# Kernel tuning notes

Measured on AMD Instinct MI355X. Metric: run time of the kernel, lower is better.

## Reference

```python
import jax, jax.numpy as jnp
import numpy as np

NE, NPER = 100000, 50000        # empresa / persona node counts
D_EMP, D_PER = 64, 32           # raw feature dims
H, OUT = 128, 64                # hidden_channels, out_channels
E_EE, E_PE, E_EP = 1600000, 800000, 800000
NEG_SLOPE = 0.2                 # GATConv leaky_relu slope


def setup_inputs() -> dict:
    key = jax.random.key(0)
    ks = jax.random.split(key, 40)

    def w(k, fi, fo):
        return jax.random.normal(k, (fi, fo), jnp.float32) / jnp.sqrt(jnp.float32(fi))

    def b(k, n):
        return jax.random.normal(k, (n,), jnp.float32) * 0.02

    return {
        "x_emp": jax.random.normal(ks[0], (NE, D_EMP), jnp.float32),
        "x_per": jax.random.normal(ks[1], (NPER, D_PER), jnp.float32),
        "ee_src": jax.random.randint(ks[2], (E_EE,), 0, NE, jnp.int32),
        "ee_dst": jax.random.randint(ks[3], (E_EE,), 0, NE, jnp.int32),
        "pe_src": jax.random.randint(ks[4], (E_PE,), 0, NPER, jnp.int32),
        "pe_dst": jax.random.randint(ks[5], (E_PE,), 0, NE, jnp.int32),
        "ep_src": jax.random.randint(ks[6], (E_EP,), 0, NE, jnp.int32),
        "ep_dst": jax.random.randint(ks[7], (E_EP,), 0, NPER, jnp.int32),
        # per-node-type input projections
        "lin_emp_w": w(ks[8], D_EMP, H), "lin_emp_b": b(ks[9], H),
        "lin_per_w": w(ks[10], D_PER, H), "lin_per_b": b(ks[11], H),
        # conv1: SAGEConv per edge type (H -> H)
        "s1_ee_Wl": w(ks[12], H, H), "s1_ee_bl": b(ks[13], H), "s1_ee_Wr": w(ks[14], H, H),
        "s1_pe_Wl": w(ks[15], H, H), "s1_pe_bl": b(ks[16], H), "s1_pe_Wr": w(ks[17], H, H),
        "s1_ep_Wl": w(ks[18], H, H), "s1_ep_bl": b(ks[19], H), "s1_ep_Wr": w(ks[20], H, H),
        # conv2: GATConv on empresa->empresa (H -> OUT, heads=1)
        "gat_Wsrc": w(ks[21], H, OUT), "gat_Wdst": w(ks[22], H, OUT),
        "gat_asrc": b(ks[23], OUT), "gat_adst": b(ks[24], OUT), "gat_b": b(ks[25], OUT),
        # conv2: SAGEConv on remaining edge types (H -> OUT)
        "s2_pe_Wl": w(ks[26], H, OUT), "s2_pe_bl": b(ks[27], OUT), "s2_pe_Wr": w(ks[28], H, OUT),
        "s2_ep_Wl": w(ks[29], H, OUT), "s2_ep_bl": b(ks[30], OUT), "s2_ep_Wr": w(ks[31], H, OUT),
    }


def _sage(h_src, h_dst, src, dst, Wl, bl, Wr, n_dst):
    # SAGEConv: mean-aggregate neighbor features, then lin_l(agg) + lin_r(x_dst)
    agg = jax.ops.segment_sum(h_src[src], dst, num_segments=n_dst)
    cnt = jax.ops.segment_sum(jnp.ones((src.shape[0], 1), h_src.dtype), dst,
                              num_segments=n_dst)
    mean = agg / jnp.maximum(cnt, 1.0)  # isolated nodes -> 0 (PyG mean behavior)
    return mean @ Wl + bl + h_dst @ Wr


def _gat(h, src, dst, Wsrc, Wdst, asrc, adst, bias, n):
    # GATConv, heads=1, no self loops: edge-softmax attention over dst neighborhoods
    zs = h @ Wsrc                                   # [n, OUT]
    zd = h @ Wdst
    e = (zs @ asrc)[src] + (zd @ adst)[dst]         # [E] attention logits
    e = jnp.where(e > 0, e, NEG_SLOPE * e)          # leaky_relu(0.2)
    m = jax.ops.segment_max(e, dst, num_segments=n)
    ex = jnp.exp(e - m[dst])
    den = jax.ops.segment_sum(ex, dst, num_segments=n)
    alpha = ex / den[dst]                           # softmax per dst node
    out = jax.ops.segment_sum(zs[src] * alpha[:, None], dst, num_segments=n)
    return out + bias


def reference(x_emp, x_per, ee_src, ee_dst, pe_src, pe_dst, ep_src, ep_dst,
              lin_emp_w, lin_emp_b, lin_per_w, lin_per_b,
              s1_ee_Wl, s1_ee_bl, s1_ee_Wr,
              s1_pe_Wl, s1_pe_bl, s1_pe_Wr,
              s1_ep_Wl, s1_ep_bl, s1_ep_Wr,
              gat_Wsrc, gat_Wdst, gat_asrc, gat_adst, gat_b,
              s2_pe_Wl, s2_pe_bl, s2_pe_Wr,
              s2_ep_Wl, s2_ep_bl, s2_ep_Wr):
    # per-node-type input Linear + relu
    h_emp = jax.nn.relu(x_emp @ lin_emp_w + lin_emp_b)
    h_per = jax.nn.relu(x_per @ lin_per_w + lin_per_b)

    # conv1: HeteroConv of SAGEConvs, aggr='sum' across relations per dst type
    emp1 = (_sage(h_emp, h_emp, ee_src, ee_dst, s1_ee_Wl, s1_ee_bl, s1_ee_Wr, NE)
            + _sage(h_per, h_emp, pe_src, pe_dst, s1_pe_Wl, s1_pe_bl, s1_pe_Wr, NE))
    per1 = _sage(h_emp, h_per, ep_src, ep_dst, s1_ep_Wl, s1_ep_bl, s1_ep_Wr, NPER)
    emp1 = jax.nn.relu(emp1)
    per1 = jax.nn.relu(per1)

    # conv2: GAT on empresa->empresa, SAGE elsewhere, sum across relations
    emp2 = (_gat(emp1, ee_src, ee_dst, gat_Wsrc, gat_Wdst, gat_asrc, gat_adst, gat_b, NE)
            + _sage(per1, emp1, pe_src, pe_dst, s2_pe_Wl, s2_pe_bl, s2_pe_Wr, NE))
    per2 = _sage(emp1, per1, ep_src, ep_dst, s2_ep_Wl, s2_ep_bl, s2_ep_Wr, NPER)
    return emp2, per2
```

## Files before the change

kernel.cpp:

```cpp
#include <hip/hip_runtime.h>
#include <cstdint>

#define NE_N   100000
#define NPER_N 50000
#define HD     128
#define OUTD   64
#define NEE    1600000
#define NPE    800000
#define NEP    800000
#define ETOT   (NEE+NPE+NEP)

static inline int ceil_div(long long a, long long b){ return (int)((a + b - 1)/b); }

__device__ __forceinline__ float4 ld4(const float* p){ return *reinterpret_cast<const float4*>(p); }
__device__ __forceinline__ void st4(float* p, float4 v){ *reinterpret_cast<float4*>(p) = v; }
__device__ __forceinline__ uint16_t f2b(float f){
    uint32_t u = __float_as_uint(f);
    u += 0x7fffu + ((u >> 16) & 1u);
    return (uint16_t)(u >> 16);
}
__device__ __forceinline__ float b2f(uint32_t u){ return __uint_as_float(u << 16); }

typedef short v8s __attribute__((ext_vector_type(8)));
typedef float v4f __attribute__((ext_vector_type(4)));

struct Seg { const uint16_t* W; const float* b; void* C; int ldw; int ldc; int mode; };
struct Segs { Seg s[6]; };

template<int K>
__global__ __launch_bounds__(256)
void gemm_mfma(const uint16_t* __restrict__ A, int N, Segs segs)
{
    constexpr int NKS  = K / 32;
    constexpr int PADK = K + 8;
    __shared__ __align__(16) uint16_t Wt[64 * PADK];

    Seg sg = segs.s[blockIdx.y];

    const int t = threadIdx.x;
// ... 40 lines not shown
    }
#pragma unroll
    for (int rt=0;rt<4;rt++){
#pragma unroll
        for (int rg=0;rg<4;rg++){
            int r = rowbase + rt*16 + lg*4 + rg;
            if (r < N){
#pragma unroll
                for (int ct=0;ct<4;ct++){
                    float v = acc[rt][ct][rg];
                    int c = ct*16 + l16;
                    if (mode == 0)
                        ((float*)sg.C)[(size_t)r*ldc + c] = v + bias[ct];
                    else if (mode == 1)
                        ((uint16_t*)sg.C)[(size_t)r*ldc + c] = f2b(v);
                    else
                        ((uint16_t*)sg.C)[(size_t)r*ldc + c] = f2b(fmaxf(v + bias[ct], 0.f));
                }
            }
        }
    }
}

__global__ void count_sharded(const int* __restrict__ ee, const int* __restrict__ pe,
                              const int* __restrict__ ep, int* __restrict__ cnt){
    int r = blockIdx.x & 7;
    int i = (blockIdx.x >> 3)*256 + threadIdx.x;
    int d, base, n;
    if (i < NEE){ d = ee[i]; base = 0; n = NE_N; }
    else if (i < NEE+NPE){ d = pe[i-NEE]; base = 100000; n = NE_N; }
    else if (i < ETOT){ d = ep[i-NEE-NPE]; base = 200000; n = NPER_N; }
    else return;
    int seg = n >> 3;
    if (d >= r*seg && d < (r+1)*seg) atomicAdd(&cnt[base + d], 1);
}
__global__ __launch_bounds__(256)
void scan_block3(const int* __restrict__ cnt_all, int* __restrict__ ee_off,
                 int* __restrict__ pe_off, int* __restrict__ ep_off,
                 int* __restrict__ partial){
    int r = blockIdx.y;
    const int* cnt = cnt_all + (r==0 ? 0 : (r==1 ? 100000 : 200000));
    int* off = (r==0) ? ee_off : (r==1 ? pe_off : ep_off);
    int n = (r==2) ? NPER_N : NE_N;
    int* part = partial + r*128;

    __shared__ int sh[256];
    int t = threadIdx.x;
    int base = blockIdx.x*1024 + t*4;
    int v0 = (base  <n)?cnt[base  ]:0;
// ... 39 lines not shown
        if (k < NPER_N) ep_off[k] += partial[256 + (k>>10)];
        else if (k == NPER_N) ep_off[NPER_N] = NEP;
    }
}
__global__ void fill_sharded(const int* __restrict__ ee_src, const int* __restrict__ ee_dst,
                             const int* __restrict__ pe_src, const int* __restrict__ pe_dst,
                             const int* __restrict__ ep_src, const int* __restrict__ ep_dst,
                             const int* __restrict__ ee_off, const int* __restrict__ pe_off,
                             const int* __restrict__ ep_off, int* __restrict__ cnt_all,
                             int* __restrict__ ee_csr, int* __restrict__ pe_csr,
                             int* __restrict__ ep_csr){
    int r = blockIdx.x & 7;
    int i = (blockIdx.x >> 3)*256 + threadIdx.x;
    int d, base, n;
    const int* srcp; const int* offp; int* csrp;
    if (i < NEE){ d = ee_dst[i]; base = 0; n = NE_N; srcp = ee_src; offp = ee_off; csrp = ee_csr; }
    else if (i < NEE+NPE){ i -= NEE; d = pe_dst[i]; base = 100000; n = NE_N; srcp = pe_src; offp = pe_off; csrp = pe_csr; }
    else if (i < ETOT){ i -= NEE+NPE; d = ep_dst[i]; base = 200000; n = NPER_N; srcp = ep_src; offp = ep_off; csrp = ep_csr; }
    else return;
    int seg = n >> 3;
    if (d >= r*seg && d < (r+1)*seg){
        int old = atomicAdd(&cnt_all[base + d], -1);
        csrp[offp[d] + old - 1] = srcp[i];
    }
}

__global__ __launch_bounds__(256)
void agg_emp1(const uint16_t* __restrict__ proj_ee, const uint16_t* __restrict__ proj_pe,
              const int* __restrict__ ee_off, const int* __restrict__ ee_csr,
              const int* __restrict__ pe_off, const int* __restrict__ pe_csr,
              const float* __restrict__ emp1f, uint16_t* __restrict__ emp1b){
    int w    = (blockIdx.x*blockDim.x + threadIdx.x) >> 6;
    int lane = threadIdx.x & 63;
    if (w >= NE_N) return;
    int grp = lane >> 4, l16 = lane & 15;

    float a[8] = {0,0,0,0,0,0,0,0};
    int b = ee_off[w], e = ee_off[w+1];
    int dee = e - b;
    for (int cb=b; cb<e; cb+=64){
        int j = cb + lane;
        int s = (j<e) ? ee_csr[j] : -1;
        int lim = e - cb; if (lim > 64) lim = 64;
        int iters = (lim + 3) >> 2;
        for (int k=0;k<iters;k++){
            int sg = __shfl(s, k*4 + grp, 64);
            if (sg >= 0){
                uint4 u = *reinterpret_cast<const uint4*>(&proj_ee[(size_t)sg*128 + l16*8]);
                a[0]+=b2f(u.x&0xffffu); a[1]+=b2f(u.x>>16);
                a[2]+=b2f(u.y&0xffffu); a[3]+=b2f(u.y>>16);
                a[4]+=b2f(u.z&0xffffu); a[5]+=b2f(u.z>>16);
                a[6]+=b2f(u.w&0xffffu); a[7]+=b2f(u.w>>16);
            }
        }
    }
    float c[8] = {0,0,0,0,0,0,0,0};
    b = pe_off[w]; e = pe_off[w+1];
    int dpe = e - b;
    for (int cb=b; cb<e; cb+=64){
        int j = cb + lane;
        int s = (j<e) ? pe_csr[j] : -1;
        int lim = e - cb; if (lim > 64) lim = 64;
        int iters = (lim + 3) >> 2;
        for (int k=0;k<iters;k++){
            int sg = __shfl(s, k*4 + grp, 64);
            if (sg >= 0){
                uint4 u = *reinterpret_cast<const uint4*>(&proj_pe[(size_t)sg*128 + l16*8]);
                c[0]+=b2f(u.x&0xffffu); c[1]+=b2f(u.x>>16);
                c[2]+=b2f(u.y&0xffffu); c[3]+=b2f(u.y>>16);
                c[4]+=b2f(u.z&0xffffu); c[5]+=b2f(u.z>>16);
                c[6]+=b2f(u.w&0xffffu); c[7]+=b2f(u.w>>16);
            }
        }
    }
#pragma unroll
    for (int f=0;f<8;f++){
        a[f] += __shfl_xor(a[f],16,64); a[f] += __shfl_xor(a[f],32,64);
        c[f] += __shfl_xor(c[f],16,64); c[f] += __shfl_xor(c[f],32,64);
    }
    if (grp == 0){
        float s1f = 1.f/fmaxf((float)dee,1.f);
        float s2f = 1.f/fmaxf((float)dpe,1.f);
        float4 e0 = ld4(&emp1f[(size_t)w*128 + l16*8]);
        float4 e1 = ld4(&emp1f[(size_t)w*128 + l16*8 + 4]);
        float o[8];
        o[0]=fmaxf(e0.x + a[0]*s1f + c[0]*s2f, 0.f);
        o[1]=fmaxf(e0.y + a[1]*s1f + c[1]*s2f, 0.f);
        o[2]=fmaxf(e0.z + a[2]*s1f + c[2]*s2f, 0.f);
        o[3]=fmaxf(e0.w + a[3]*s1f + c[3]*s2f, 0.f);
        o[4]=fmaxf(e1.x + a[4]*s1f + c[4]*s2f, 0.f);
        o[5]=fmaxf(e1.y + a[5]*s1f + c[5]*s2f, 0.f);
        o[6]=fmaxf(e1.z + a[6]*s1f + c[6]*s2f, 0.f);
        o[7]=fmaxf(e1.w + a[7]*s1f + c[7]*s2f, 0.f);
        uint4 pk;
        pk.x = (uint32_t)f2b(o[0]) | ((uint32_t)f2b(o[1])<<16);
        pk.y = (uint32_t)f2b(o[2]) | ((uint32_t)f2b(o[3])<<16);
        pk.z = (uint32_t)f2b(o[4]) | ((uint32_t)f2b(o[5])<<16);
        pk.w = (uint32_t)f2b(o[6]) | ((uint32_t)f2b(o[7])<<16);
        *reinterpret_cast<uint4*>(&emp1b[(size_t)w*128 + l16*8]) = pk;
    }
}
__global__ __launch_bounds__(256)
void agg_per1(const uint16_t* __restrict__ proj_ep,
              const int* __restrict__ ep_off, const int* __restrict__ ep_csr,
              const float* __restrict__ per1f, uint16_t* __restrict__ per1b){
    int w    = (blockIdx.x*blockDim.x + threadIdx.x) >> 6;
    int lane = threadIdx.x & 63;
    if (w >= NPER_N) return;
    int grp = lane >> 4, l16 = lane & 15;

    float a[8] = {0,0,0,0,0,0,0,0};
    int b = ep_off[w], e = ep_off[w+1];
    int deg = e - b;
    for (int cb=b; cb<e; cb+=64){
        int j = cb + lane;
        int s = (j<e) ? ep_csr[j] : -1;
        int lim = e - cb; if (lim > 64) lim = 64;
        int iters = (lim + 3) >> 2;
        for (int k=0;k<iters;k++){
            int sg = __shfl(s, k*4 + grp, 64);
            if (sg >= 0){
                uint4 u = *reinterpret_cast<const uint4*>(&proj_ep[(size_t)sg*128 + l16*8]);
                a[0]+=b2f(u.x&0xffffu); a[1]+=b2f(u.x>>16);
                a[2]+=b2f(u.y&0xffffu); a[3]+=b2f(u.y>>16);
                a[4]+=b2f(u.z&0xffffu); a[5]+=b2f(u.z>>16);
                a[6]+=b2f(u.w&0xffffu); a[7]+=b2f(u.w>>16);
            }
        }
    }
#pragma unroll
    for (int f=0;f<8;f++){
        a[f] += __shfl_xor(a[f],16,64); a[f] += __shfl_xor(a[f],32,64);
    }
    if (grp == 0){
        float s1f = 1.f/fmaxf((float)deg,1.f);
        float4 e0 = ld4(&per1f[(size_t)w*128 + l16*8]);
        float4 e1 = ld4(&per1f[(size_t)w*128 + l16*8 + 4]);
        float o[8];
        o[0]=fmaxf(e0.x + a[0]*s1f, 0.f); o[1]=fmaxf(e0.y + a[1]*s1f, 0.f);
        o[2]=fmaxf(e0.z + a[2]*s1f, 0.f); o[3]=fmaxf(e0.w + a[3]*s1f, 0.f);
        o[4]=fmaxf(e1.x + a[4]*s1f, 0.f); o[5]=fmaxf(e1.y + a[5]*s1f, 0.f);
        o[6]=fmaxf(e1.z + a[6]*s1f, 0.f); o[7]=fmaxf(e1.w + a[7]*s1f, 0.f);
        uint4 pk;
        pk.x = (uint32_t)f2b(o[0]) | ((uint32_t)f2b(o[1])<<16);
        pk.y = (uint32_t)f2b(o[2]) | ((uint32_t)f2b(o[3])<<16);
        pk.z = (uint32_t)f2b(o[4]) | ((uint32_t)f2b(o[5])<<16);
        pk.w = (uint32_t)f2b(o[6]) | ((uint32_t)f2b(o[7])<<16);
        *reinterpret_cast<uint4*>(&per1b[(size_t)w*128 + l16*8]) = pk;
    }
}
__global__ __launch_bounds__(256)
void agg_per2(const uint16_t* __restrict__ p2ep,
              const int* __restrict__ ep_off, const int* __restrict__ ep_csr,
              float* __restrict__ out){
    int w    = (blockIdx.x*blockDim.x + threadIdx.x) >> 6;
    int lane = threadIdx.x & 63;
    if (w >= NPER_N) return;
    int grp = lane >> 4, l16 = lane & 15;

    float a[4] = {0,0,0,0};
    int b = ep_off[w], e = ep_off[w+1];
    int deg = e - b;
    for (int cb=b; cb<e; cb+=64){
        int j = cb + lane;
        int s = (j<e) ? ep_csr[j] : -1;
        int lim = e - cb; if (lim > 64) lim = 64;
        int iters = (lim + 3) >> 2;
        for (int k=0;k<iters;k++){
            int sg = __shfl(s, k*4 + grp, 64);
            if (sg >= 0){
                uint2 u = *reinterpret_cast<const uint2*>(&p2ep[(size_t)sg*64 + l16*4]);
                a[0]+=b2f(u.x&0xffffu); a[1]+=b2f(u.x>>16);
                a[2]+=b2f(u.y&0xffffu); a[3]+=b2f(u.y>>16);
            }
        }
    }
#pragma unroll
    for (int f=0;f<4;f++){
        a[f] += __shfl_xor(a[f],16,64); a[f] += __shfl_xor(a[f],32,64);
    }
    if (grp == 0){
        float s1f = 1.f/fmaxf((float)deg,1.f);
        float4 o4 = ld4(&out[(size_t)w*64 + l16*4]);
        o4.x += a[0]*s1f; o4.y += a[1]*s1f; o4.z += a[2]*s1f; o4.w += a[3]*s1f;
        st4(&out[(size_t)w*64 + l16*4], o4);
    }
}
__global__ __launch_bounds__(256)
void gat_sage_emp2(const int* __restrict__ ee_off, const int* __restrict__ ee_csr,
                   const int* __restrict__ pe_off, const int* __restrict__ pe_csr,
                   const float* __restrict__ as, const float* __restrict__ ad,
                   const uint16_t* __restrict__ zs, const uint16_t* __restrict__ p2pe,
                   float* __restrict__ out){
    int w    = (blockIdx.x*blockDim.x + threadIdx.x) >> 6;
    int lane = threadIdx.x & 63;
    if (w >= NE_N) return;
    int grp = lane >> 4, l16 = lane & 15;

    float g[4] = {0,0,0,0};
    float invden = 0.f;
    int b = ee_off[w], e = ee_off[w+1];
    if (e > b){
        float add = ad[w];
        float m = -INFINITY;
        for (int j=b+lane; j<e; j+=64){
            float ev = as[ee_csr[j]] + add;
            ev = ev > 0.f ? ev : 0.2f*ev;
            m = fmaxf(m, ev);
        }
        for (int o=32;o;o>>=1) m = fmaxf(m, __shfl_xor(m,o,64));

        float den = 0.f;
        for (int cb=b; cb<e; cb+=64){
            int j = cb + lane;
            int s = 0; float ex = 0.f;
            if (j < e){
                s = ee_csr[j];
                float ev = as[s] + add;
                ev = ev > 0.f ? ev : 0.2f*ev;
                ex = expf(ev - m);
            }
            den += ex;
            int lim = e - cb; if (lim > 64) lim = 64;
            int iters = (lim + 3) >> 2;
            for (int k=0;k<iters;k++){
                int   sg = __shfl(s,  k*4 + grp, 64);
                float ag = __shfl(ex, k*4 + grp, 64);
                uint2 u = *reinterpret_cast<const uint2*>(&zs[(size_t)sg*64 + l16*4]);
                g[0] += ag*b2f(u.x&0xffffu); g[1] += ag*b2f(u.x>>16);
                g[2] += ag*b2f(u.y&0xffffu); g[3] += ag*b2f(u.y>>16);
            }
        }
        for (int o=32;o;o>>=1) den += __shfl_xor(den,o,64);
        invden = 1.f/den;
    }

    float p[4] = {0,0,0,0};
    b = pe_off[w]; e = pe_off[w+1];
    int deg = e - b;
    for (int cb=b; cb<e; cb+=64){
        int j = cb + lane;
        int s = (j<e) ? pe_csr[j] : -1;
        int lim = e - cb; if (lim > 64) lim = 64;
        int iters = (lim + 3) >> 2;
        for (int k=0;k<iters;k++){
            int sg = __shfl(s, k*4 + grp, 64);
            if (sg >= 0){
                uint2 u = *reinterpret_cast<const uint2*>(&p2pe[(size_t)sg*64 + l16*4]);
                p[0]+=b2f(u.x&0xffffu); p[1]+=b2f(u.x>>16);
                p[2]+=b2f(u.y&0xffffu); p[3]+=b2f(u.y>>16);
            }
        }
    }
#pragma unroll
    for (int f=0;f<4;f++){
        g[f] += __shfl_xor(g[f],16,64); g[f] += __shfl_xor(g[f],32,64);
        p[f] += __shfl_xor(p[f],16,64); p[f] += __shfl_xor(p[f],32,64);
    }
    if (grp == 0){
        float s2f = 1.f/fmaxf((float)deg,1.f);
        float4 o4 = ld4(&out[(size_t)w*64 + l16*4]);
        o4.x += g[0]*invden + p[0]*s2f;
        o4.y += g[1]*invden + p[1]*s2f;
        o4.z += g[2]*invden + p[2]*s2f;
        o4.w += g[3]*invden + p[3]*s2f;
        st4(&out[(size_t)w*64 + l16*4], o4);
    }
}

__global__ void rowdots(const uint16_t* __restrict__ ZS, const uint16_t* __restrict__ E1,
                        const float* __restrict__ wa, const float* __restrict__ wv,
                        float* __restrict__ a_s, float* __restrict__ a_d){
    int wid  = (blockIdx.x*blockDim.x + threadIdx.x) >> 6;
    int lane = threadIdx.x & 63;
    if (wid < NE_N){
        float v = b2f((uint32_t)ZS[(size_t)wid*64 + lane])*wa[lane];
        for (int o=32;o;o>>=1) v += __shfl_xor(v,o,64);
        if (lane==0) a_s[wid]=v;
    } else if (wid < 2*NE_N){
        int k = wid - NE_N;
        float v = b2f((uint32_t)E1[(size_t)k*128 + lane])*wv[lane]
// ... 51 lines not shown
        case 6:  src=linp_w; dst=wb+WB_LINP;   n=4096;  break;
        case 7:  src=gatW;   dst=wb+WB_GATW;   n=8192;  break;
        case 8:  src=s2epWl; dst=wb+WB_S2EPWL; n=8192;  break;
        case 9:  src=s2peWr; dst=wb+WB_S2PEWR; n=8192;  break;
        case 10: src=s2peWl; dst=wb+WB_S2PEWL; n=8192;  break;
        default: src=s2epWr; dst=wb+WB_S2EPWR; n=8192;  break;
    }
    for (int i=t; i<n; i+=256) dst[i] = f2b(src[i]);
}

__global__ void convx(const float* __restrict__ xe, const float* __restrict__ xp,
                      uint16_t* __restrict__ be, uint16_t* __restrict__ bp){
    const int NE4 = NE_N*64/4, NP4 = NPER_N*32/4;
    int i = blockIdx.x*blockDim.x + threadIdx.x;
    if (i < NE4){
        float4 v = ld4(xe + (size_t)i*4);
        uint2 o;
        o.x = (uint32_t)f2b(v.x) | ((uint32_t)f2b(v.y) << 16);
        o.y = (uint32_t)f2b(v.z) | ((uint32_t)f2b(v.w) << 16);
        *reinterpret_cast<uint2*>(&be[(size_t)i*4]) = o;
    } else if (i < NE4 + NP4){
        int k = i - NE4;
        float4 v = ld4(xp + (size_t)k*4);
        uint2 o;
        o.x = (uint32_t)f2b(v.x) | ((uint32_t)f2b(v.y) << 16);
        o.y = (uint32_t)f2b(v.z) | ((uint32_t)f2b(v.w) << 16);
        *reinterpret_cast<uint2*>(&bp[(size_t)k*4]) = o;
    }
}

constexpr size_t OFF_R0 = 0;
constexpr size_t OFF_R1 = 3200000;
constexpr size_t OFF_R2 = 4800000;
constexpr size_t OFF_R3 = 11200000;
constexpr size_t OFF_R4 = 14400000;
constexpr size_t OFF_R5 = 27200000;
constexpr size_t OFF_R6 = 33600000;
constexpr size_t OFF_R7 = 40000000;
// ... 33 lines not shown
    const float* gat_Wsrc=(const float*)d_in[21], *gat_Wdst=(const float*)d_in[22];
    const float* gat_asrc=(const float*)d_in[23], *gat_adst=(const float*)d_in[24], *gat_b=(const float*)d_in[25];
    const float* s2_pe_Wl=(const float*)d_in[26], *s2_pe_bl=(const float*)d_in[27], *s2_pe_Wr=(const float*)d_in[28];
    const float* s2_ep_Wl=(const float*)d_in[29], *s2_ep_bl=(const float*)d_in[30], *s2_ep_Wr=(const float*)d_in[31];

    float* ws = (float*)d_ws;
    int*   wi = (int*)d_ws;
    float* out_emp = (float*)d_out;
    float* out_per = out_emp + (size_t)NE_N*OUTD;

    uint16_t* xbe     = (uint16_t*)(ws + OFF_R0);
    uint16_t* zsB     = (uint16_t*)(ws + OFF_R0);
    uint16_t* xbp     = (uint16_t*)(ws + OFF_R1);
    uint16_t* p2peB   = (uint16_t*)(ws + OFF_R1);
    uint16_t* h_empB  = (uint16_t*)(ws + OFF_R2);
    uint16_t* emp1B   = (uint16_t*)(ws + OFF_R2);
    uint16_t* h_perB  = (uint16_t*)(ws + OFF_R3);
    uint16_t* per1B   = (uint16_t*)(ws + OFF_R3);
    float*    emp1F   = ws + OFF_R4;
    uint16_t* p2epB   = (uint16_t*)(ws + OFF_R4);
    float*    per1F   = ws + OFF_R5;
    uint16_t* proj_eeB= (uint16_t*)(ws + OFF_R6);
    uint16_t* proj_peB= (uint16_t*)(ws + OFF_R7);
    uint16_t* proj_epB= (uint16_t*)(ws + OFF_R8);
    float* a_s   = ws + OFF_AS;
    float* a_d   = ws + OFF_AD;
    uint16_t* WB = (uint16_t*)(ws + OFF_WB);
    float* bsum1 = ws + OFF_BS1;
    float* b2sum = ws + OFF_BS2;
    float* vvec  = ws + OFF_VV;

    int* cnt_all = wi + OFF_CNT;
    int* ee_off = wi + OFF_EE_OFF; int* ee_csr = wi + OFF_EE_CSR;
    int* pe_off = wi + OFF_PE_OFF; int* pe_csr = wi + OFF_PE_CSR;
    int* ep_off = wi + OFF_EP_OFF; int* ep_csr = wi + OFF_EP_CSR;
    int* part   = wi + OFF_PART;

    const int GE = ceil_div(NE_N,256), GP = ceil_div(NPER_N,256);

    hipMemsetAsync(cnt_all, 0, 250000*sizeof(int), stream);

    prep<<<13,256,0,stream>>>(s1_ee_Wr, s1_pe_Wr, s1_ee_Wl, s1_ep_Wl, s1_pe_Wl, s1_ep_Wr,
                              lin_emp_w, lin_per_w,
                              gat_Wsrc, s2_ep_Wl, s2_pe_Wr, s2_pe_Wl, s2_ep_Wr,
                              s1_ee_bl, s1_pe_bl, s2_pe_bl, gat_b, gat_Wdst, gat_adst,
                              WB, bsum1, b2sum, vvec);
    convx<<<ceil_div(NE_N*64/4 + NPER_N*32/4, 256),256,0,stream>>>(x_emp, x_per, xbe, xbp);

    const int NCHUNK = ceil_div(ETOT,256);
    count_sharded<<<NCHUNK*8,256,0,stream>>>(ee_dst, pe_dst, ep_dst, cnt_all);
    scan_block3<<<dim3(ceil_div(NE_N,1024),3),256,0,stream>>>(cnt_all, ee_off, pe_off, ep_off, part);
    scan_partial3<<<3,64,0,stream>>>(part);
    add_base3<<<ceil_div(2*(NE_N+1)+NPER_N+1,256),256,0,stream>>>(ee_off, pe_off, ep_off, part);
    fill_sharded<<<NCHUNK*8,256,0,stream>>>(ee_src, ee_dst, pe_src, pe_dst, ep_src, ep_dst,
                                            ee_off, pe_off, ep_off, cnt_all,
                                            ee_csr, pe_csr, ep_csr);

    {
        Segs g{};
        g.s[0] = Seg{WB+WB_LINE,    lin_emp_b,    (void*)h_empB,      128,128,2};
        g.s[1] = Seg{WB+WB_LINE+64, lin_emp_b+64, (void*)(h_empB+64), 128,128,2};
        g.s[2]=g.s[0]; g.s[3]=g.s[0]; g.s[4]=g.s[0]; g.s[5]=g.s[0];
        gemm_mfma<64><<<dim3(GE,2),256,0,stream>>>(xbe, NE_N, g);
    }
    {
        Segs g{};
        g.s[0] = Seg{WB+WB_LINP,    lin_per_b,    (void*)h_perB,      128,128,2};
        g.s[1] = Seg{WB+WB_LINP+64, lin_per_b+64, (void*)(h_perB+64), 128,128,2};
        g.s[2]=g.s[0]; g.s[3]=g.s[0]; g.s[4]=g.s[0]; g.s[5]=g.s[0];
        gemm_mfma<32><<<dim3(GP,2),256,0,stream>>>(xbp, NPER_N, g);
    }
    {
        Segs g{};
        g.s[0] = Seg{WB+WB_WSUM,    bsum1,    (void*)emp1F,        128,128,0};
        g.s[1] = Seg{WB+WB_WSUM+64, bsum1+64, (void*)(emp1F+64),   128,128,0};
        g.s[2] = Seg{WB+WB_EEWL,    nullptr,  (void*)proj_eeB,     128,128,1};
        g.s[3] = Seg{WB+WB_EEWL+64, nullptr,  (void*)(proj_eeB+64),128,128,1};
        g.s[4] = Seg{WB+WB_EPWL,    nullptr,  (void*)proj_epB,     128,128,1};
        g.s[5] = Seg{WB+WB_EPWL+64, nullptr,  (void*)(proj_epB+64),128,128,1};
        gemm_mfma<128><<<dim3(GE,6),256,0,stream>>>(h_empB, NE_N, g);
    }
    {
        Segs g{};
        g.s[0] = Seg{WB+WB_PEWL,    nullptr,     (void*)proj_peB,     128,128,1};
        g.s[1] = Seg{WB+WB_PEWL+64, nullptr,     (void*)(proj_peB+64),128,128,1};
        g.s[2] = Seg{WB+WB_EPWR1,   s1_ep_bl,    (void*)per1F,        128,128,0};
        g.s[3] = Seg{WB+WB_EPWR1+64,s1_ep_bl+64, (void*)(per1F+64),   128,128,0};
        g.s[4]=g.s[0]; g.s[5]=g.s[0];
        gemm_mfma<128><<<dim3(GP,4),256,0,stream>>>(h_perB, NPER_N, g);
    }
    agg_emp1<<<ceil_div((long long)NE_N*64,256),256,0,stream>>>(proj_eeB, proj_peB, ee_off, ee_csr, pe_off, pe_csr, emp1F, emp1B);
    agg_per1<<<ceil_div((long long)NPER_N*64,256),256,0,stream>>>(proj_epB, ep_off, ep_csr, per1F, per1B);

    {
        Segs g{};
        g.s[0] = Seg{WB+WB_GATW,   nullptr, (void*)zsB,     64,64,1};
        g.s[1] = Seg{WB+WB_S2EPWL, nullptr, (void*)p2epB,   64,64,1};
        g.s[2] = Seg{WB+WB_S2PEWR, b2sum,   (void*)out_emp, 64,64,0};
        g.s[3]=g.s[0]; g.s[4]=g.s[0]; g.s[5]=g.s[0];
        gemm_mfma<128><<<dim3(GE,3),256,0,stream>>>(emp1B, NE_N, g);
    }
    rowdots<<<ceil_div(2*NE_N,4),256,0,stream>>>(zsB, emp1B, gat_asrc, vvec, a_s, a_d);
    {
        Segs g{};
        g.s[0] = Seg{WB+WB_S2PEWL, nullptr,  (void*)p2peB,   64,64,1};
        g.s[1] = Seg{WB+WB_S2EPWR, s2_ep_bl, (void*)out_per, 64,64,0};
        g.s[2]=g.s[0]; g.s[3]=g.s[0]; g.s[4]=g.s[0]; g.s[5]=g.s[0];
        gemm_mfma<128><<<dim3(GP,2),256,0,stream>>>(per1B, NPER_N, g);
    }

    gat_sage_emp2<<<ceil_div((long long)NE_N*64,256),256,0,stream>>>(ee_off, ee_csr, pe_off, pe_csr, a_s, a_d, zsB, p2peB, out_emp);
    agg_per2<<<ceil_div((long long)NPER_N*64,256),256,0,stream>>>(p2epB, ep_off, ep_csr, out_per);
}
```

Baseline: 797.5 us.

## Fuse per-type aggregation kernels, store self terms in bf16, unshard degree counting

After: 1.083 ms. +35.8%, slower.

```diff
diff --git a/kernel.cpp b/kernel.cpp
--- a/kernel.cpp
+++ b/kernel.cpp
@@ -23,6 +23,8 @@
 
 typedef short v8s __attribute__((ext_vector_type(8)));
 typedef float v4f __attribute__((ext_vector_type(4)));
+typedef unsigned int v4u __attribute__((ext_vector_type(4)));
+typedef float v4fl __attribute__((ext_vector_type(4)));
 
 struct Seg { const uint16_t* W; const float* b; void* C; int ldw; int ldc; int mode; };
 struct Segs { Seg s[6]; };
@@ -93,25 +95,22 @@
                         ((float*)sg.C)[(size_t)r*ldc + c] = v + bias[ct];
                     else if (mode == 1)
                         ((uint16_t*)sg.C)[(size_t)r*ldc + c] = f2b(v);
+                    else if (mode == 2)
+                        ((uint16_t*)sg.C)[(size_t)r*ldc + c] = f2b(fmaxf(v + bias[ct], 0.f));
                     else
-                        ((uint16_t*)sg.C)[(size_t)r*ldc + c] = f2b(fmaxf(v + bias[ct], 0.f));
+                        ((uint16_t*)sg.C)[(size_t)r*ldc + c] = f2b(v + bias[ct]);
                 }
             }
         }
     }
 }
 
-__global__ void count_sharded(const int* __restrict__ ee, const int* __restrict__ pe,
-                              const int* __restrict__ ep, int* __restrict__ cnt){
-    int r = blockIdx.x & 7;
-    int i = (blockIdx.x >> 3)*256 + threadIdx.x;
-    int d, base, n;
-    if (i < NEE){ d = ee[i]; base = 0; n = NE_N; }
-    else if (i < NEE+NPE){ d = pe[i-NEE]; base = 100000; n = NE_N; }
-    else if (i < ETOT){ d = ep[i-NEE-NPE]; base = 200000; n = NPER_N; }
-    else return;
-    int seg = n >> 3;
-    if (d >= r*seg && d < (r+1)*seg) atomicAdd(&cnt[base + d], 1);
+__global__ void count_all(const int* __restrict__ ee, const int* __restrict__ pe,
+                          const int* __restrict__ ep, int* __restrict__ cnt){
+    int i = blockIdx.x*blockDim.x + threadIdx.x;
+    if (i < NEE) atomicAdd(&cnt[__builtin_nontemporal_load(&ee[i])], 1);
+    else if (i < NEE+NPE) atomicAdd(&cnt[100000 + __builtin_nontemporal_load(&pe[i-NEE])], 1);
+    else if (i < ETOT) atomicAdd(&cnt[200000 + __builtin_nontemporal_load(&ep[i-NEE-NPE])], 1);
 }
 __global__ __launch_bounds__(256)
 void scan_block3(const int* __restrict__ cnt_all, int* __restrict__ ee_off,
@@ -181,257 +180,239 @@
     int i = (blockIdx.x >> 3)*256 + threadIdx.x;
     int d, base, n;
     const int* srcp; const int* offp; int* csrp;
-    if (i < NEE){ d = ee_dst[i]; base = 0; n = NE_N; srcp = ee_src; offp = ee_off; csrp = ee_csr; }
-    else if (i < NEE+NPE){ i -= NEE; d = pe_dst[i]; base = 100000; n = NE_N; srcp = pe_src; offp = pe_off; csrp = pe_csr; }
-    else if (i < ETOT){ i -= NEE+NPE; d = ep_dst[i]; base = 200000; n = NPER_N; srcp = ep_src; offp = ep_off; csrp = ep_csr; }
+    if (i < NEE){ d = __builtin_nontemporal_load(&ee_dst[i]); base = 0; n = NE_N; srcp = ee_src; offp = ee_off; csrp = ee_csr; }
+    else if (i < NEE+NPE){ i -= NEE; d = __builtin_nontemporal_load(&pe_dst[i]); base = 100000; n = NE_N; srcp = pe_src; offp = pe_off; csrp = pe_csr; }
+    else if (i < ETOT){ i -= NEE+NPE; d = __builtin_nontemporal_load(&ep_dst[i]); base = 200000; n = NPER_N; srcp = ep_src; offp = ep_off; csrp = ep_csr; }
     else return;
     int seg = n >> 3;
     if (d >= r*seg && d < (r+1)*seg){
         int old = atomicAdd(&cnt_all[base + d], -1);
-        csrp[offp[d] + old - 1] = srcp[i];
-    }
-}
-
-__global__ __launch_bounds__(256)
-void agg_emp1(const uint16_t* __restrict__ proj_ee, const uint16_t* __restrict__ proj_pe,
-              const int* __restrict__ ee_off, const int* __restrict__ ee_csr,
-              const int* __restrict__ pe_off, const int* __restrict__ pe_csr,
-              const float* __restrict__ emp1f, uint16_t* __restrict__ emp1b){
-    int w    = (blockIdx.x*blockDim.x + threadIdx.x) >> 6;
-    int lane = threadIdx.x & 63;
-    if (w >= NE_N) return;
-    int grp = lane >> 4, l16 = lane & 15;
-
-    float a[8] = {0,0,0,0,0,0,0,0};
-    int b = ee_off[w], e = ee_off[w+1];
-    int dee = e - b;
-    for (int cb=b; cb<e; cb+=64){
+        csrp[offp[d] + old - 1] = __builtin_nontemporal_load(&srcp[i]);
+    }
+}
+
+__device__ __forceinline__ void gadd128(float* acc, const uint16_t* __restrict__ proj,
+                                        int sg, int l16){
+    uint4 u = *reinterpret_cast<const uint4*>(&proj[(size_t)sg*128 + l16*8]);
+    acc[0]+=b2f(u.x&0xffffu); acc[1]+=b2f(u.x>>16);
+    acc[2]+=b2f(u.y&0xffffu); acc[3]+=b2f(u.y>>16);
+    acc[4]+=b2f(u.z&0xffffu); acc[5]+=b2f(u.z>>16);
+    acc[6]+=b2f(u.w&0xffffu); acc[7]+=b2f(u.w>>16);
+}
+__device__ __forceinline__ void gather128(const uint16_t* __restrict__ proj,
+                                          const int* __restrict__ csr,
+                                          int b, int e, int lane, int grp, int l16,
+                                          float* acc){
+    int nfull = (e - b) >> 6;
+    for (int cc=0; cc<nfull; cc++){
+        int s = __builtin_nontemporal_load(&csr[b + cc*64 + lane]);
+#pragma unroll
+        for (int k=0;k<16;k++) gadd128(acc, proj, __shfl(s, k*4 + grp, 64), l16);
+    }
+    int cb = b + nfull*64;
+    if (cb < e){
         int j = cb + lane;
-        int s = (j<e) ? ee_csr[j] : -1;
-        int lim = e - cb; if (lim > 64) lim = 64;
-        int iters = (lim + 3) >> 2;
+        int s = (j<e) ? __builtin_nontemporal_load(&csr[j]) : -1;
+        int iters = (e - cb + 3) >> 2;
         for (int k=0;k<iters;k++){
             int sg = __shfl(s, k*4 + grp, 64);
-            if (sg >= 0){
-                uint4 u = *reinterpret_cast<const uint4*>(&proj_ee[(size_t)sg*128 + l16*8]);
-                a[0]+=b2f(u.x&0xffffu); a[1]+=b2f(u.x>>16);
-                a[2]+=b2f(u.y&0xffffu); a[3]+=b2f(u.y>>16);
-                a[4]+=b2f(u.z&0xffffu); a[5]+=b2f(u.z>>16);
-                a[6]+=b2f(u.w&0xffffu); a[7]+=b2f(u.w>>16);
-            }
-        }
-    }
-    float c[8] = {0,0,0,0,0,0,0,0};
-    b = pe_off[w]; e = pe_off[w+1];
-    int dpe = e - b;
-    for (int cb=b; cb<e; cb+=64){
+            if (sg >= 0) gadd128(acc, proj, sg, l16);
+        }
+    }
+}
+__device__ __forceinline__ void gadd64(float* acc, const uint16_t* __restrict__ proj,
+                                       int sg, int l16){
+    uint2 u = *reinterpret_cast<const uint2*>(&proj[(size_t)sg*64 + l16*4]);
+    acc[0]+=b2f(u.x&0xffffu); acc[1]+=b2f(u.x>>16);
+    acc[2]+=b2f(u.y&0xffffu); acc[3]+=b2f(u.y>>16);
+}
+__device__ __forceinline__ void gather64(const uint16_t* __restrict__ proj,
+                                         const int* __restrict__ csr,
+                                         int b, int e, int lane, int grp, int l16,
+                                         float* acc){
+    int nfull = (e - b) >> 6;
+    for (int cc=0; cc<nfull; cc++){
+        int s = __builtin_nontemporal_load(&csr[b + cc*64 + lane]);
+#pragma unroll
+        for (int k=0;k<16;k++) gadd64(acc, proj, __shfl(s, k*4 + grp, 64), l16);
+    }
+    int cb = b + nfull*64;
+    if (cb < e){
         int j = cb + lane;
-        int s = (j<e) ? pe_csr[j] : -1;
-        int lim = e - cb; if (lim > 64) lim = 64;
-        int iters = (lim + 3) >> 2;
+        int s = (j<e) ? __builtin_nontemporal_load(&csr[j]) : -1;
+        int iters = (e - cb + 3) >> 2;
         for (int k=0;k<iters;k++){
             int sg = __shfl(s, k*4 + grp, 64);
-            if (sg >= 0){
-                uint4 u = *reinterpret_cast<const uint4*>(&proj_pe[(size_t)sg*128 + l16*8]);
-                c[0]+=b2f(u.x&0xffffu); c[1]+=b2f(u.x>>16);
-                c[2]+=b2f(u.y&0xffffu); c[3]+=b2f(u.y>>16);
-                c[4]+=b2f(u.z&0xffffu); c[5]+=b2f(u.z>>16);
-                c[6]+=b2f(u.w&0xffffu); c[7]+=b2f(u.w>>16);
+            if (sg >= 0) gadd64(acc, proj, sg, l16);
+        }
+    }
+}
+
+__global__ __launch_bounds__(256)
+void agg1_fused(const uint16_t* __restrict__ proj_ee, const uint16_t* __restrict__ proj_pe,
+                const uint16_t* __restrict__ proj_ep,
+                const int* __restrict__ ee_off, const int* __restrict__ ee_csr,
+                const int* __restrict__ pe_off, const int* __restrict__ pe_csr,
+                const int* __restrict__ ep_off, const int* __restrict__ ep_csr,
+                uint16_t* __restrict__ emp1b, uint16_t* __restrict__ per1b){
+    int gw   = (blockIdx.x*blockDim.x + threadIdx.x) >> 6;
+    int lane = threadIdx.x & 63;
+    int grp = lane >> 4, l16 = lane & 15;
+
+    if (gw < NE_N){
+        int w = gw;
+        float a[8] = {0,0,0,0,0,0,0,0};
+        float c[8] = {0,0,0,0,0,0,0,0};
+        int b0 = ee_off[w], e0 = ee_off[w+1];
+        int b1 = pe_off[w], e1 = pe_off[w+1];
+        gather128(proj_ee, ee_csr, b0, e0, lane, grp, l16, a);
+        gather128(proj_pe, pe_csr, b1, e1, lane, grp, l16, c);
+#pragma unroll
+        for (int f=0;f<8;f++){
+            a[f] += __shfl_xor(a[f],16,64); a[f] += __shfl_xor(a[f],32,64);
+            c[f] += __shfl_xor(c[f],16,64); c[f] += __shfl_xor(c[f],32,64);
+        }
+        if (grp == 0){
+            float s1f = 1.f/fmaxf((float)(e0-b0),1.f);
+            float s2f = 1.f/fmaxf((float)(e1-b1),1.f);
+            v4u sb = __builtin_nontemporal_load(
+                reinterpret_cast<const v4u*>(&emp1b[(size_t)w*128 + l16*8]));
+            float sf[8] = { b2f(sb.x&0xffffu), b2f(sb.x>>16), b2f(sb.y&0xffffu), b2f(sb.y>>16),
+                            b2f(sb.z&0xffffu), b2f(sb.z>>16), b2f(sb.w&0xffffu), b2f(sb.w>>16) };
+            uint4 pk;
+            uint32_t o[8];
+#pragma unroll
+            for (int f=0;f<8;f++) o[f] = (uint32_t)f2b(fmaxf(sf[f] + a[f]*s1f + c[f]*s2f, 0.f));
+            pk.x = o[0] | (o[1]<<16); pk.y = o[2] | (o[3]<<16);
+            pk.z = o[4] | (o[5]<<16); pk.w = o[6] | (o[7]<<16);
+            *reinterpret_cast<uint4*>(&emp1b[(size_t)w*128 + l16*8]) = pk;
+        }
+    } else if (gw < NE_N + NPER_N){
+        int w = gw - NE_N;
+        float a[8] = {0,0,0,0,0,0,0,0};
+        int b0 = ep_off[w], e0 = ep_off[w+1];
+        gather128(proj_ep, ep_csr, b0, e0, lane, grp, l16, a);
+#pragma unroll
+        for (int f=0;f<8;f++){
+            a[f] += __shfl_xor(a[f],16,64); a[f] += __shfl_xor(a[f],32,64);
+        }
+        if (grp == 0){
+            float s1f = 1.f/fmaxf((float)(e0-b0),1.f);
+            v4u sb = __builtin_nontemporal_load(
+                reinterpret_cast<const v4u*>(&per1b[(size_t)w*128 + l16*8]));
+            float sf[8] = { b2f(sb.x&0xffffu), b2f(sb.x>>16), b2f(sb.y&0xffffu), b2f(sb.y>>16),
+                            b2f(sb.z&0xffffu), b2f(sb.z>>16), b2f(sb.w&0xffffu), b2f(sb.w>>16) };
+            uint4 pk;
+            uint32_t o[8];
+#pragma unroll
+            for (int f=0;f<8;f++) o[f] = (uint32_t)f2b(fmaxf(sf[f] + a[f]*s1f, 0.f));
+            pk.x = o[0] | (o[1]<<16); pk.y = o[2] | (o[3]<<16);
+            pk.z = o[4] | (o[5]<<16); pk.w = o[6] | (o[7]<<16);
+            *reinterpret_cast<uint4*>(&per1b[(size_t)w*128 + l16*8]) = pk;
+        }
+    }
+}
+
+__global__ __launch_bounds__(256)
+void agg2_fused(const int* __restrict__ ee_off, const int* __restrict__ ee_csr,
+                const int* __restrict__ pe_off, const int* __restrict__ pe_csr,
+                const int* __restrict__ ep_off, const int* __restrict__ ep_csr,
+                const float* __restrict__ as, const float* __restrict__ ad,
+                const uint16_t* __restrict__ zs, const uint16_t* __restrict__ p2pe,
+                const uint16_t* __restrict__ p2ep,
+                float* __restrict__ out_emp, float* __restrict__ out_per){
+    int gw   = (blockIdx.x*blockDim.x + threadIdx.x) >> 6;
+    int lane = threadIdx.x & 63;
+    int grp = lane >> 4, l16 = lane & 15;
+
+    if (gw < NE_N){
+        int w = gw;
+        float g[4] = {0,0,0,0};
+        float invden = 0.f;
+        int b = ee_off[w], e = ee_off[w+1];
+        if (e > b){
+            float add = ad[w];
+            float m = -INFINITY;
+            for (int j=b+lane; j<e; j+=64){
+                float ev = as[ee_csr[j]] + add;
+                ev = ev > 0.f ? ev : 0.2f*ev;
+                m = fmaxf(m, ev);
             }
-        }
-    }
-#pragma unroll
-    for (int f=0;f<8;f++){
-        a[f] += __shfl_xor(a[f],16,64); a[f] += __shfl_xor(a[f],32,64);
-        c[f] += __shfl_xor(c[f],16,64); c[f] += __shfl_xor(c[f],32,64);
-    }
-    if (grp == 0){
-        float s1f = 1.f/fmaxf((float)dee,1.f);
-        float s2f = 1.f/fmaxf((float)dpe,1.f);
-        float4 e0 = ld4(&emp1f[(size_t)w*128 + l16*8]);
-        float4 e1 = ld4(&emp1f[(size_t)w*128 + l16*8 + 4]);
-        float o[8];
-        o[0]=fmaxf(e0.x + a[0]*s1f + c[0]*s2f, 0.f);
-        o[1]=fmaxf(e0.y + a[1]*s1f + c[1]*s2f, 0.f);
-        o[2]=fmaxf(e0.z + a[2]*s1f + c[2]*s2f, 0.f);
-        o[3]=fmaxf(e0.w + a[3]*s1f + c[3]*s2f, 0.f);
-        o[4]=fmaxf(e1.x + a[4]*s1f + c[4]*s2f, 0.f);
-        o[5]=fmaxf(e1.y + a[5]*s1f + c[5]*s2f, 0.f);
-        o[6]=fmaxf(e1.z + a[6]*s1f + c[6]*s2f, 0.f);
-        o[7]=fmaxf(e1.w + a[7]*s1f + c[7]*s2f, 0.f);
-        uint4 pk;
-        pk.x = (uint32_t)f2b(o[0]) | ((uint32_t)f2b(o[1])<<16);
-        pk.y = (uint32_t)f2b(o[2]) | ((uint32_t)f2b(o[3])<<16);
-        pk.z = (uint32_t)f2b(o[4]) | ((uint32_t)f2b(o[5])<<16);
-        pk.w = (uint32_t)f2b(o[6]) | ((uint32_t)f2b(o[7])<<16);
-        *reinterpret_cast<uint4*>(&emp1b[(size_t)w*128 + l16*8]) = pk;
-    }
-}
-__global__ __launch_bounds__(256)
-void agg_per1(const uint16_t* __restrict__ proj_ep,
-              const int* __restrict__ ep_off, const int* __restrict__ ep_csr,
-              const float* __restrict__ per1f, uint16_t* __restrict__ per1b){
-    int w    = (blockIdx.x*blockDim.x + threadIdx.x) >> 6;
-    int lane = threadIdx.x & 63;
-    if (w >= NPER_N) return;
-    int grp = lane >> 4, l16 = lane & 15;
-
-    float a[8] = {0,0,0,0,0,0,0,0};
-    int b = ep_off[w], e = ep_off[w+1];
-    int deg = e - b;
-    for (int cb=b; cb<e; cb+=64){
-        int j = cb + lane;
-        int s = (j<e) ? ep_csr[j] : -1;
-        int lim = e - cb; if (lim > 64) lim = 64;
-        int iters = (lim + 3) >> 2;
-        for (int k=0;k<iters;k++){
-            int sg = __shfl(s, k*4 + grp, 64);
-            if (sg >= 0){
-                uint4 u = *reinterpret_cast<const uint4*>(&proj_ep[(size_t)sg*128 + l16*8]);
-                a[0]+=b2f(u.x&0xffffu); a[1]+=b2f(u.x>>16);
-                a[2]+=b2f(u.y&0xffffu); a[3]+=b2f(u.y>>16);
-                a[4]+=b2f(u.z&0xffffu); a[5]+=b2f(u.z>>16);
-                a[6]+=b2f(u.w&0xffffu); a[7]+=b2f(u.w>>16);
-            }
-        }
-    }
-#pragma unroll
-    for (int f=0;f<8;f++){
-        a[f] += __shfl_xor(a[f],16,64); a[f] += __shfl_xor(a[f],32,64);
-    }
-    if (grp == 0){
-        float s1f = 1.f/fmaxf((float)deg,1.f);
-        float4 e0 = ld4(&per1f[(size_t)w*128 + l16*8]);
-        float4 e1 = ld4(&per1f[(size_t)w*128 + l16*8 + 4]);
-        float o[8];
-        o[0]=fmaxf(e0.x + a[0]*s1f, 0.f); o[1]=fmaxf(e0.y + a[1]*s1f, 0.f);
-        o[2]=fmaxf(e0.z + a[2]*s1f, 0.f); o[3]=fmaxf(e0.w + a[3]*s1f, 0.f);
-        o[4]=fmaxf(e1.x + a[4]*s1f, 0.f); o[5]=fmaxf(e1.y + a[5]*s1f, 0.f);
-        o[6]=fmaxf(e1.z + a[6]*s1f, 0.f); o[7]=fmaxf(e1.w + a[7]*s1f, 0.f);
-        uint4 pk;
-        pk.x = (uint32_t)f2b(o[0]) | ((uint32_t)f2b(o[1])<<16);
-        pk.y = (uint32_t)f2b(o[2]) | ((uint32_t)f2b(o[3])<<16);
-        pk.z = (uint32_t)f2b(o[4]) | ((uint32_t)f2b(o[5])<<16);
-        pk.w = (uint32_t)f2b(o[6]) | ((uint32_t)f2b(o[7])<<16);
-        *reinterpret_cast<uint4*>(&per1b[(size_t)w*128 + l16*8]) = pk;
-    }
-}
-__global__ __launch_bounds__(256)
-void agg_per2(const uint16_t* __restrict__ p2ep,
-              const int* __restrict__ ep_off, const int* __restrict__ ep_csr,
-              float* __restrict__ out){
-    int w    = (blockIdx.x*blockDim.x + threadIdx.x) >> 6;
-    int lane = threadIdx.x & 63;
-    if (w >= NPER_N) return;
-    int grp = lane >> 4, l16 = lane & 15;
-
-    float a[4] = {0,0,0,0};
-    int b = ep_off[w], e = ep_off[w+1];
-    int deg = e - b;
-    for (int cb=b; cb<e; cb+=64){
-        int j = cb + lane;
-        int s = (j<e) ? ep_csr[j] : -1;
-        int lim = e - cb; if (lim > 64) lim = 64;
-        int iters = (lim + 3) >> 2;
-        for (int k=0;k<iters;k++){
-            int sg = __shfl(s, k*4 + grp, 64);
-            if (sg >= 0){
-                uint2 u = *reinterpret_cast<const uint2*>(&p2ep[(size_t)sg*64 + l16*4]);
-                a[0]+=b2f(u.x&0xffffu); a[1]+=b2f(u.x>>16);
-                a[2]+=b2f(u.y&0xffffu); a[3]+=b2f(u.y>>16);
-            }
-        }
-    }
-#pragma unroll
-    for (int f=0;f<4;f++){
-        a[f] += __shfl_xor(a[f],16,64); a[f] += __shfl_xor(a[f],32,64);
-    }
-    if (grp == 0){
-        float s1f = 1.f/fmaxf((float)deg,1.f);
-        float4 o4 = ld4(&out[(size_t)w*64 + l16*4]);
-        o4.x += a[0]*s1f; o4.y += a[1]*s1f; o4.z += a[2]*s1f; o4.w += a[3]*s1f;
-        st4(&out[(size_t)w*64 + l16*4], o4);
-    }
-}
-__global__ __launch_bounds__(256)
-void gat_sage_emp2(const int* __restrict__ ee_off, const int* __restrict__ ee_csr,
-                   const int* __restrict__ pe_off, const int* __restrict__ pe_csr,
-                   const float* __restrict__ as, const float* __restrict__ ad,
-                   const uint16_t* __restrict__ zs, const uint16_t* __restrict__ p2pe,
-                   float* __restrict__ out){
-    int w    = (blockIdx.x*blockDim.x + threadIdx.x) >> 6;
-    int lane = threadIdx.x & 63;
-    if (w >= NE_N) return;
-    int grp = lane >> 4, l16 = lane & 15;
-
-    float g[4] = {0,0,0,0};
-    float invden = 0.f;
-    int b = ee_off[w], e = ee_off[w+1];
-    if (e > b){
-        float add = ad[w];
-        float m = -INFINITY;
-        for (int j=b+lane; j<e; j+=64){
-            float ev = as[ee_csr[j]] + add;
-            ev = ev > 0.f ? ev : 0.2f*ev;
-            m = fmaxf(m, ev);
-        }
-        for (int o=32;o;o>>=1) m = fmaxf(m, __shfl_xor(m,o,64));
-
-        float den = 0.f;
-        for (int cb=b; cb<e; cb+=64){
-            int j = cb + lane;
-            int s = 0; float ex = 0.f;
-            if (j < e){
-                s = ee_csr[j];
+            for (int o=32;o;o>>=1) m = fmaxf(m, __shfl_xor(m,o,64));
+
+            float den = 0.f;
+            int nfull = (e - b) >> 6;
+            for (int cc=0; cc<nfull; cc++){
+                int s = ee_csr[b + cc*64 + lane];
                 float ev = as[s] + add;
                 ev = ev > 0.f ? ev : 0.2f*ev;
-                ex = expf(ev - m);
+                float ex = expf(ev - m);
+                den += ex;
+#pragma unroll
+                for (int k=0;k<16;k++){
+                    int   sg = __shfl(s,  k*4 + grp, 64);
+                    float ag = __shfl(ex, k*4 + grp, 64);
+                    uint2 u = *reinterpret_cast<const uint2*>(&zs[(size_t)sg*64 + l16*4]);
+                    g[0] += ag*b2f(u.x&0xffffu); g[1] += ag*b2f(u.x>>16);
+                    g[2] += ag*b2f(u.y&0xffffu); g[3] += ag*b2f(u.y>>16);
+                }
             }
-            den += ex;
-            int lim = e - cb; if (lim > 64) lim = 64;
-            int iters = (lim + 3) >> 2;
-            for (int k=0;k<iters;k++){
-                int   sg = __shfl(s,  k*4 + grp, 64);
-                float ag = __shfl(ex, k*4 + grp, 64);
-                uint2 u = *reinterpret_cast<const uint2*>(&zs[(size_t)sg*64 + l16*4]);
-                g[0] += ag*b2f(u.x&0xffffu); g[1] += ag*b2f(u.x>>16);
-                g[2] += ag*b2f(u.y&0xffffu); g[3] += ag*b2f(u.y>>16);
+            int cb = b + nfull*64;
+            if (cb < e){
+                int j = cb + lane;
+                int s = 0; float ex = 0.f;
+                if (j < e){
+                    s = ee_csr[j];
+                    float ev = as[s] + add;
+                    ev = ev > 0.f ? ev : 0.2f*ev;
+                    ex = expf(ev - m);
+                }
+                den += ex;
+                int iters = (e - cb + 3) >> 2;
+                for (int k=0;k<iters;k++){
+                    int   sg = __shfl(s,  k*4 + grp, 64);
+                    float ag = __shfl(ex, k*4 + grp, 64);
+                    uint2 u = *reinterpret_cast<const uint2*>(&zs[(size_t)sg*64 + l16*4]);
+                    g[0] += ag*b2f(u.x&0xffffu); g[1] += ag*b2f(u.x>>16);
+                    g[2] += ag*b2f(u.y&0xffffu); g[3] += ag*b2f(u.y>>16);
+                }
             }
-        }
-        for (int o=32;o;o>>=1) den += __shfl_xor(den,o,64);
-        invden = 1.f/den;
-    }
-
-    float p[4] = {0,0,0,0};
-    b = pe_off[w]; e = pe_off[w+1];
-    int deg = e - b;
-    for (int cb=b; cb<e; cb+=64){
-        int j = cb + lane;
-        int s = (j<e) ? pe_csr[j] : -1;
-        int lim = e - cb; if (lim > 64) lim = 64;
-        int iters = (lim + 3) >> 2;
-        for (int k=0;k<iters;k++){
-            int sg = __shfl(s, k*4 + grp, 64);
-            if (sg >= 0){
-                uint2 u = *reinterpret_cast<const uint2*>(&p2pe[(size_t)sg*64 + l16*4]);
-                p[0]+=b2f(u.x&0xffffu); p[1]+=b2f(u.x>>16);
-                p[2]+=b2f(u.y&0xffffu); p[3]+=b2f(u.y>>16);
-            }
-        }
-    }
-#pragma unroll
-    for (int f=0;f<4;f++){
-        g[f] += __shfl_xor(g[f],16,64); g[f] += __shfl_xor(g[f],32,64);
-        p[f] += __shfl_xor(p[f],16,64); p[f] += __shfl_xor(p[f],32,64);
-    }
-    if (grp == 0){
-        float s2f = 1.f/fmaxf((float)deg,1.f);
-        float4 o4 = ld4(&out[(size_t)w*64 + l16*4]);
-        o4.x += g[0]*invden + p[0]*s2f;
-        o4.y += g[1]*invden + p[1]*s2f;
-        o4.z += g[2]*invden + p[2]*s2f;
-        o4.w += g[3]*invden + p[3]*s2f;
-        st4(&out[(size_t)w*64 + l16*4], o4);
+            for (int o=32;o;o>>=1) den += __shfl_xor(den,o,64);
+            invden = 1.f/den;
+        }
+
+        float p[4] = {0,0,0,0};
+        b = pe_off[w]; e = pe_off[w+1];
+        gather64(p2pe, pe_csr, b, e, lane, grp, l16, p);
+#pragma unroll
+        for (int f=0;f<4;f++){
+            g[f] += __shfl_xor(g[f],16,64); g[f] += __shfl_xor(g[f],32,64);
+            p[f] += __shfl_xor(p[f],16,64); p[f] += __shfl_xor(p[f],32,64);
+        }
+        if (grp == 0){
+            float s2f = 1.f/fmaxf((float)(e-b),1.f);
+            float4 o4 = ld4(&out_emp[(size_t)w*64 + l16*4]);
+            o4.x += g[0]*invden + p[0]*s2f;
+            o4.y += g[1]*invden + p[1]*s2f;
+            o4.z += g[2]*invden + p[2]*s2f;
+            o4.w += g[3]*invden + p[3]*s2f;
+            st4(&out_emp[(size_t)w*64 + l16*4], o4);
+        }
+    } else if (gw < NE_N + NPER_N){
+        int w = gw - NE_N;
+        float a[4] = {0,0,0,0};
+        int b = ep_off[w], e = ep_off[w+1];
+        gather64(p2ep, ep_csr, b, e, lane, grp, l16, a);
+#pragma unroll
+        for (int f=0;f<4;f++){
+            a[f] += __shfl_xor(a[f],16,64); a[f] += __shfl_xor(a[f],32,64);
+        }
+        if (grp == 0){
+            float s1f = 1.f/fmaxf((float)(e-b),1.f);
+            float4 o4 = ld4(&out_per[(size_t)w*64 + l16*4]);
+            o4.x += a[0]*s1f; o4.y += a[1]*s1f; o4.z += a[2]*s1f; o4.w += a[3]*s1f;
+            st4(&out_per[(size_t)w*64 + l16*4], o4);
+        }
     }
 }
 
@@ -513,14 +494,14 @@
     const int NE4 = NE_N*64/4, NP4 = NPER_N*32/4;
     int i = blockIdx.x*blockDim.x + threadIdx.x;
     if (i < NE4){
-        float4 v = ld4(xe + (size_t)i*4);
+        v4fl v = __builtin_nontemporal_load(reinterpret_cast<const v4fl*>(xe + (size_t)i*4));
         uint2 o;
         o.x = (uint32_t)f2b(v.x) | ((uint32_t)f2b(v.y) << 16);
         o.y = (uint32_t)f2b(v.z) | ((uint32_t)f2b(v.w) << 16);
         *reinterpret_cast<uint2*>(&be[(size_t)i*4]) = o;
     } else if (i < NE4 + NP4){
         int k = i - NE4;
-        float4 v = ld4(xp + (size_t)k*4);
+        v4fl v = __builtin_nontemporal_load(reinterpret_cast<const v4fl*>(xp + (size_t)k*4));
         uint2 o;
         o.x = (uint32_t)f2b(v.x) | ((uint32_t)f2b(v.y) << 16);
         o.y = (uint32_t)f2b(v.z) | ((uint32_t)f2b(v.w) << 16);
@@ -584,12 +565,10 @@
     uint16_t* xbp     = (uint16_t*)(ws + OFF_R1);
     uint16_t* p2peB   = (uint16_t*)(ws + OFF_R1);
     uint16_t* h_empB  = (uint16_t*)(ws + OFF_R2);
-    uint16_t* emp1B   = (uint16_t*)(ws + OFF_R2);
     uint16_t* h_perB  = (uint16_t*)(ws + OFF_R3);
-    uint16_t* per1B   = (uint16_t*)(ws + OFF_R3);
-    float*    emp1F   = ws + OFF_R4;
-    uint16_t* p2epB   = (uint16_t*)(ws + OFF_R4);
-    float*    per1F   = ws + OFF_R5;
+    uint16_t* emp1B   = (uint16_t*)(ws + OFF_R4);
+    uint16_t* per1B   = (uint16_t*)(ws + OFF_R4 + 6400000);
+    uint16_t* p2epB   = (uint16_t*)(ws + OFF_R5);
     uint16_t* proj_eeB= (uint16_t*)(ws + OFF_R6);
     uint16_t* proj_peB= (uint16_t*)(ws + OFF_R7);
     uint16_t* proj_epB= (uint16_t*)(ws + OFF_R8);
@@ -617,11 +596,11 @@
                               WB, bsum1, b2sum, vvec);
     convx<<<ceil_div(NE_N*64/4 + NPER_N*32/4, 256),256,0,stream>>>(x_emp, x_per, xbe, xbp);
 
-    const int NCHUNK = ceil_div(ETOT,256);
-    count_sharded<<<NCHUNK*8,256,0,stream>>>(ee_dst, pe_dst, ep_dst, cnt_all);
+    count_all<<<ceil_div(ETOT,256),256,0,stream>>>(ee_dst, pe_dst, ep_dst, cnt_all);
     scan_block3<<<dim3(ceil_div(NE_N,1024),3),256,0,stream>>>(cnt_all, ee_off, pe_off, ep_off, part);
     scan_partial3<<<3,64,0,stream>>>(part);
     add_base3<<<ceil_div(2*(NE_N+1)+NPER_N+1,256),256,0,stream>>>(ee_off, pe_off, ep_off, part);
+    const int NCHUNK = ceil_div(ETOT,256);
     fill_sharded<<<NCHUNK*8,256,0,stream>>>(ee_src, ee_dst, pe_src, pe_dst, ep_src, ep_dst,
                                             ee_off, pe_off, ep_off, cnt_all,
                                             ee_csr, pe_csr, ep_csr);
@@ -642,8 +621,8 @@
     }
     {
         Segs g{};
-        g.s[0] = Seg{WB+WB_WSUM,    bsum1,    (void*)emp1F,        128,128,0};
-        g.s[1] = Seg{WB+WB_WSUM+64, bsum1+64, (void*)(emp1F+64),   128,128,0};
+        g.s[0] = Seg{WB+WB_WSUM,    bsum1,    (void*)emp1B,        128,128,3};
+        g.s[1] = Seg{WB+WB_WSUM+64, bsum1+64, (void*)(emp1B+64),   128,128,3};
         g.s[2] = Seg{WB+WB_EEWL,    nullptr,  (void*)proj_eeB,     128,128,1};
         g.s[3] = Seg{WB+WB_EEWL+64, nullptr,  (void*)(proj_eeB+64),128,128,1};
         g.s[4] = Seg{WB+WB_EPWL,    nullptr,  (void*)proj_epB,     128,128,1};
@@ -654,13 +633,14 @@
         Segs g{};
         g.s[0] = Seg{WB+WB_PEWL,    nullptr,     (void*)proj_peB,     128,128,1};
         g.s[1] = Seg{WB+WB_PEWL+64, nullptr,     (void*)(proj_peB+64),128,128,1};
-        g.s[2] = Seg{WB+WB_EPWR1,   s1_ep_bl,    (void*)per1F,        128,128,0};
-        g.s[3] = Seg{WB+WB_EPWR1+64,s1_ep_bl+64, (void*)(per1F+64),   128,128,0};
+        g.s[2] = Seg{WB+WB_EPWR1,   s1_ep_bl,    (void*)per1B,        128,128,3};
+        g.s[3] = Seg{WB+WB_EPWR1+64,s1_ep_bl+64, (void*)(per1B+64),   128,128,3};
         g.s[4]=g.s[0]; g.s[5]=g.s[0];
         gemm_mfma<128><<<dim3(GP,4),256,0,stream>>>(h_perB, NPER_N, g);
     }
-    agg_emp1<<<ceil_div((long long)NE_N*64,256),256,0,stream>>>(proj_eeB, proj_peB, ee_off, ee_csr, pe_off, pe_csr, emp1F, emp1B);
-    agg_per1<<<ceil_div((long long)NPER_N*64,256),256,0,stream>>>(proj_epB, ep_off, ep_csr, per1F, per1B);
+    agg1_fused<<<ceil_div((long long)(NE_N+NPER_N)*64,256),256,0,stream>>>(
+        proj_eeB, proj_peB, proj_epB, ee_off, ee_csr, pe_off, pe_csr, ep_off, ep_csr,
+        emp1B, per1B);
 
     {
         Segs g{};
@@ -679,6 +659,7 @@
         gemm_mfma<128><<<dim3(GP,2),256,0,stream>>>(per1B, NPER_N, g);
     }
 
-    gat_sage_emp2<<<ceil_div((long long)NE_N*64,256),256,0,stream>>>(ee_off, ee_csr, pe_off, pe_csr, a_s, a_d, zsB, p2peB, out_emp);
-    agg_per2<<<ceil_div((long long)NPER_N*64,256),256,0,stream>>>(p2epB, ep_off, ep_csr, out_per);
-}
+    agg2_fused<<<ceil_div((long long)(NE_N+NPER_N)*64,256),256,0,stream>>>(
+        ee_off, ee_csr, pe_off, pe_csr, ep_off, ep_csr, a_s, a_d,
+        zsB, p2peB, p2epB, out_emp, out_per);
+}
```
